# Performance work log

Hardware: AMD Instinct MI355X
Metric: run time of the kernel (lower is better)

The kernel has to match this reference:

```python
import jax, jax.numpy as jnp
import numpy as np

EMB_DIM = 512
N_HEAD = 8
EPS = 1e-5


def gen_pos_emb(emb_dim, max_len):
    half = emb_dim // 2
    r = 10000.0 ** (-1.0 / half)
    freq = r ** jnp.arange(half, dtype=jnp.float32)  # cumprod of [1, r, r, ...]
    phase = jnp.arange(max_len, dtype=jnp.float32)[:, None] * freq[None, :]  # [L, half]
    pe = jnp.zeros((max_len, emb_dim), dtype=jnp.float32)
    pe = pe.at[:, 0::2].set(jnp.sin(phase)).at[:, 1::2].set(jnp.cos(phase))
    return pe  # [L, E]


def setup_inputs() -> dict:
    key = jax.random.key(0)
    ks = jax.random.split(key, 12)
    bs, L, E, H, V = 8, 2048, EMB_DIM, N_HEAD, 32000
    inputs = jax.random.randint(ks[0], (bs, L), 0, V, dtype=jnp.int64 if jax.config.jax_enable_x64 else jnp.int32)
    lens = jnp.sort(jax.random.randint(ks[1], (bs,), 1, L + 1, dtype=jnp.int32))
    lens = lens.at[-1].set(L)  # model requires lens[-1] == max_len
    s = 0.02
    emb_table = (jax.random.normal(ks[2], (V, E), jnp.float32) * s).at[0].set(0.0)  # padding_idx=0
    qkv_w = jax.random.normal(ks[3], (3 * E, E), jnp.float32) * s
    qkv_b = jax.random.normal(ks[4], (3 * E,), jnp.float32) * s
    gn_w = jnp.ones((H,), jnp.float32)
    gn_b = jnp.zeros((H,), jnp.float32)
    ln_w = jnp.ones((E,), jnp.float32)
    ln_b = jnp.zeros((E,), jnp.float32)
    w1 = jax.random.normal(ks[5], (2 * E, E), jnp.float32) * s
    b1 = jax.random.normal(ks[6], (2 * E,), jnp.float32) * s
    w2 = jax.random.normal(ks[7], (E, 2 * E), jnp.float32) * s
    b2 = jax.random.normal(ks[8], (E,), jnp.float32) * s
    return {"inputs": inputs, "lens": lens, "emb_table": emb_table, "qkv_w": qkv_w,
            "qkv_b": qkv_b, "gn_w": gn_w, "gn_b": gn_b, "ln_w": ln_w, "ln_b": ln_b,
            "w1": w1, "b1": b1, "w2": w2, "b2": b2}


def _forward(inputs, lens, emb_table, qkv_w, qkv_b, gn_w, gn_b, ln_w, ln_b, w1, b1, w2, b2):
    bs, L = inputs.shape
    E, H = EMB_DIM, N_HEAD
    dh = E // H
    scaling = (E / H) ** -0.5

    # embedding + positional encoding; torch works seq-major: emb [L, bs, E]
    emb = emb_table[inputs.T] + gen_pos_emb(E, L)[:, None, :]

    # qkv projection and head split
    qkv = emb @ qkv_w.T + qkv_b                      # [L, bs, 3E]
    qkv = qkv.reshape(L, bs * H, 3 * dh).transpose(1, 0, 2)  # [B=bs*H, L, 3dh]
    q, k, v = jnp.split(qkv, 3, axis=-1)             # each [B, L, dh]

    # attention-sum: softmax over keys with zero-score mask, then sum over queries
    scores = jnp.einsum('bqd,bkd->bqk', q, k) * scaling   # [B, L, L]
    mask = scores == 0
    aw = jax.nn.softmax(jnp.where(mask, -jnp.inf, scores), axis=-1)
    aw = jnp.where(mask, 0.0, aw).sum(axis=-2)            # [B, L]

    attn_out = jnp.einsum('bl,bld->bd', aw, v).reshape(bs, H, dh)  # [bs, H, dh]

    # GroupNorm(n_head, n_head): per-channel normalization over dh with affine
    mu = attn_out.mean(-1, keepdims=True)
    var = attn_out.var(-1, keepdims=True)
    attn_out = (attn_out - mu) * jax.lax.rsqrt(var + EPS)
    attn_out = attn_out * gn_w[None, :, None] + gn_b[None, :, None]
    ft = attn_out.reshape(bs, E)

    # post_process: residual with length-normalized sum of embeddings
    x = ft + emb.sum(0) / lens.astype(emb.dtype)[:, None]  # [bs, E]

    # LayerNorm -> Linear -> tanh -> Linear, residual
    m = x.mean(-1, keepdims=True)
    vv = x.var(-1, keepdims=True)
    xn = (x - m) * jax.lax.rsqrt(vv + EPS) * ln_w + ln_b
    ff = jnp.tanh(xn @ w1.T + b1) @ w2.T + b2
    return x + ff


def reference(inputs, lens, emb_table, qkv_w, qkv_b, gn_w, gn_b, ln_w, ln_b, w1, b1, w2, b2):
    return _forward(inputs, lens, emb_table, qkv_w, qkv_b, gn_w, gn_b, ln_w, ln_b, w1, b1, w2, b2)
```

## Files before the change

kernel.cpp:

```cpp
#include <hip/hip_runtime.h>
#include <math.h>

#define L_SEQ 2048
#define BS 8
#define EMB 512
#define NHEAD 8
#define DH 64
#define NB (BS*NHEAD)

typedef short short8  __attribute__((ext_vector_type(8)));
typedef short short4v __attribute__((ext_vector_type(4)));
typedef float f32x4   __attribute__((ext_vector_type(4)));

__device__ __forceinline__ short f2bf(float x) {
    unsigned u = __float_as_uint(x);
    unsigned r = (u + 0x7FFFu + ((u >> 16) & 1u)) >> 16;
    return (short)r;
}
__device__ __forceinline__ float bf2f(short h) {
    return __uint_as_float(((unsigned)(unsigned short)h) << 16);
}

__global__ void freq_kernel(float* __restrict__ freq) {
    int j = threadIdx.x;
    double r = pow(10000.0, -1.0 / 256.0);
    float rf = (float)r;
    freq[j] = (float)pow((double)rf, (double)j);
}

__global__ __launch_bounds__(256) void pe_kernel(const float* __restrict__ freq,
                                                 float* __restrict__ pe) {
    int l = blockIdx.x;
    int j = threadIdx.x;
    float ph = (float)l * freq[j];
    pe[l*EMB + 2*j]     = sinf(ph);
    pe[l*EMB + 2*j + 1] = cosf(ph);
}

__global__ __launch_bounds__(256) void embed_kernel(const int* __restrict__ inputs,
                                                    const float* __restrict__ table,
                                                    const float* __restrict__ pe,
                                                    float* __restrict__ emb,
                                                    short* __restrict__ ahi,
                                                    short* __restrict__ alo) {
    int idx = blockIdx.x*256 + threadIdx.x;
    int e4 = idx & 127;
    int rb = idx >> 7;
    int b  = rb & 7;
    int l  = rb >> 3;
    int tok = inputs[b*L_SEQ + l];
    float4 tv = reinterpret_cast<const float4*>(table)[(size_t)tok*128 + e4];
    float4 pv = reinterpret_cast<const float4*>(pe)[(size_t)l*128 + e4];
    float4 o;
    o.x = tv.x + pv.x; o.y = tv.y + pv.y; o.z = tv.z + pv.z; o.w = tv.w + pv.w;
    reinterpret_cast<float4*>(emb)[(size_t)rb*128 + e4] = o;
    int e0   = e4 * 4;
    int tile = rb >> 4;
    int ks   = e0 >> 5;
    int lane = (rb & 15) + (((e0 >> 3) & 3) << 4);
    int j0   = e0 & 7;
    size_t off = ((((size_t)tile*16 + ks) << 6) + lane)*8 + j0;
    float v[4] = {o.x, o.y, o.z, o.w};
    short4v h4, l4;
    #pragma unroll
    for (int q = 0; q < 4; q++) {
        short hb = f2bf(v[q]);
        h4[q] = hb;
        l4[q] = f2bf(v[q] - bf2f(hb));
    }
    *reinterpret_cast<short4v*>(ahi + off) = h4;
    *reinterpret_cast<short4v*>(alo + off) = l4;
}

__global__ __launch_bounds__(256) void embsum_kernel(const float* __restrict__ emb,
                                                     float* __restrict__ embsum) {
    int b  = blockIdx.x;
    int ec = blockIdx.y;
    int lc = blockIdx.z;
    int e  = ec*256 + threadIdx.x;
    float s = 0.f;
    int l0 = lc*128;
    for (int l = l0; l < l0+128; l++)
        s += emb[((size_t)l*BS + b)*EMB + e];
    atomicAdd(&embsum[b*EMB + e], s);
}

__global__ __launch_bounds__(256) void wsplit_kernel(const float* __restrict__ src,
                                                     short8* __restrict__ hi,
                                                     short8* __restrict__ lo) {
    int idx = blockIdx.x*256 + threadIdx.x;
    int c = idx & 63;
    int r = idx >> 6;
    const float4* s4 = reinterpret_cast<const float4*>(src + (size_t)r*512 + c*8);
    float4 f0 = s4[0], f1 = s4[1];
    int ks   = c >> 2;
    int lane = (r & 15) + ((c & 3) << 4);
    int tile = r >> 4;
    float v[8] = {f0.x,f0.y,f0.z,f0.w,f1.x,f1.y,f1.z,f1.w};
    short8 h8, l8;
    #pragma unroll
    for (int q = 0; q < 8; q++) {
        short hb = f2bf(v[q]);
        h8[q] = hb;
        l8[q] = f2bf(v[q] - bf2f(hb));
    }
    size_t o = (((size_t)tile*16 + ks) << 6) + lane;
    hi[o] = h8; lo[o] = l8;
}

__global__ __launch_bounds__(256) void qkv_mfma_kernel(const short8* __restrict__ ahi,
                                                       const short8* __restrict__ alo,
                                                       const short8* __restrict__ bhi,
                                                       const short8* __restrict__ blo,
                                                       const float* __restrict__ bias,
                                                       short* __restrict__ qh,
                                                       short* __restrict__ kh,
                                                       float* __restrict__ vg) {
    __shared__ short8 sA[2][8][64];
    __shared__ short8 sB[2][8][64];
    int id  = blockIdx.x;
    int xcd = id & 7, pos = id >> 3;
    int nb  = pos % 12;
    int mb  = xcd*16 + pos/12;
    int t  = threadIdx.x;
    int w  = t >> 6, lane = t & 63;
    int wr = w >> 1, wc = w & 1;

    f32x4 acc[4][4];
    #pragma unroll
    for (int i = 0; i < 4; i++)
        #pragma unroll
        for (int j = 0; j < 4; j++)
            acc[i][j] = (f32x4){0.f, 0.f, 0.f, 0.f};

    short8 stg[8];
    #pragma unroll
    for (int i = 0; i < 8; i++) {
        int li = w*8 + i;
        int h = li & 1, ti = (li >> 1) & 7, isB = li >> 4;
        const short8* base = isB ? (h ? blo : bhi) : (h ? alo : ahi);
        int gt = isB ? (nb*8 + ti) : (mb*8 + ti);
        stg[i] = base[(((size_t)gt*16 + 0) << 6) + lane];
    }
    for (int ks = 0; ks < 16; ks++) {
        __syncthreads();
        #pragma unroll
        for (int i = 0; i < 8; i++) {
            int li = w*8 + i;
            int h = li & 1, ti = (li >> 1) & 7, isB = li >> 4;
            if (isB) sB[h][ti][lane] = stg[i];
            else     sA[h][ti][lane] = stg[i];
        }
        __syncthreads();
        if (ks < 15) {
            #pragma unroll
            for (int i = 0; i < 8; i++) {
                int li = w*8 + i;
                int h = li & 1, ti = (li >> 1) & 7, isB = li >> 4;
                const short8* base = isB ? (h ? blo : bhi) : (h ? alo : ahi);
                int gt = isB ? (nb*8 + ti) : (mb*8 + ti);
                stg[i] = base[(((size_t)gt*16 + (ks+1)) << 6) + lane];
            }
        }
        short8 Ah[4], Al[4];
        #pragma unroll
        for (int fi = 0; fi < 4; fi++) {
            Ah[fi] = sA[0][wr*4 + fi][lane];
            Al[fi] = sA[1][wr*4 + fi][lane];
        }
        #pragma unroll
        for (int fj = 0; fj < 4; fj++) {
            short8 Bh = sB[0][wc*4 + fj][lane];
            short8 Bl = sB[1][wc*4 + fj][lane];
            #pragma unroll
            for (int fi = 0; fi < 4; fi++) {
                acc[fi][fj] = __builtin_amdgcn_mfma_f32_16x16x32_bf16(Ah[fi], Bh, acc[fi][fj], 0, 0, 0);
                acc[fi][fj] = __builtin_amdgcn_mfma_f32_16x16x32_bf16(Ah[fi], Bl, acc[fi][fj], 0, 0, 0);
                acc[fi][fj] = __builtin_amdgcn_mfma_f32_16x16x32_bf16(Al[fi], Bh, acc[fi][fj], 0, 0, 0);
            }
        }
    }
    int row0 = (lane >> 4) * 4;
    int col  = lane & 15;
    #pragma unroll
    for (int fj = 0; fj < 4; fj++) {
        int n   = nb*128 + wc*64 + fj*16 + col;
        int h   = n / 192;
        int sel = (n % 192) / 64;
        float bn = bias[n];
        int nn = n & 63;
        #pragma unroll
        for (int fi = 0; fi < 4; fi++) {
            int m0 = mb*128 + wr*64 + fi*16 + row0;
            #pragma unroll
            for (int r = 0; r < 4; r++) {
                int m = m0 + r;
                int l = m >> 3, b = m & 7;
                size_t o = (((size_t)(b*NHEAD + h))*L_SEQ + l)*DH + nn;
                float val = acc[fi][fj][r] + bn;
                if (sel == 2)      vg[o] = val;
                else if (sel == 1) kh[o] = f2bf(val);
                else               qh[o] = f2bf(val);
            }
        }
    }
}

__global__ __launch_bounds__(256) void reformat16_kernel(const short* __restrict__ src,
                                                         short8* __restrict__ dst) {
    int idx = blockIdx.x*256 + threadIdx.x;
    int c  = idx & 7;
    int r  = (idx >> 3) & 2047;
    int bh = idx >> 14;
    short8 v = *reinterpret_cast<const short8*>(src + ((size_t)bh*L_SEQ + r)*DH + c*8);
    int ks   = c >> 2;
    int lane = (r & 15) + ((c & 3) << 4);
    int tile = r >> 4;
    dst[(((size_t)(bh*128 + tile)*2 + ks) << 6) + lane] = v;
}

__global__ __launch_bounds__(256) void ml_mfma_kernel(const short8* __restrict__ qbf,
                                                      const short8* __restrict__ kbf,
                                                      float* __restrict__ cq) {
    int bh = blockIdx.x, wv = threadIdx.x >> 6, lane = threadIdx.x & 63;
    int qt0 = (blockIdx.y*4 + wv)*4;
    short8 bq0[4], bq1[4];
    #pragma unroll
    for (int j = 0; j < 4; j++) {
        const short8* qp = qbf + (((size_t)(bh*128 + qt0 + j)*2) << 6) + lane;
        bq0[j] = qp[0]; bq1[j] = qp[64];
    }
    const short8* kp = kbf + ((size_t)bh << 14) + lane;
    float lsum[4] = {0.f, 0.f, 0.f, 0.f};
    for (int t = 0; t < 128; t++) {
        short8 a0 = kp[0], a1 = kp[64];
        kp += 128;
        #pragma unroll
        for (int j = 0; j < 4; j++) {
            f32x4 acc = {0.f, 0.f, 0.f, 0.f};
            acc = __builtin_amdgcn_mfma_f32_16x16x32_bf16(a0, bq0[j], acc, 0, 0, 0);
            acc = __builtin_amdgcn_mfma_f32_16x16x32_bf16(a1, bq1[j], acc, 0, 0, 0);
            #pragma unroll
            for (int r = 0; r < 4; r++)
                lsum[j] += (acc[r] != 0.f) ? __expf(acc[r]*0.125f) : 0.f;
        }
    }
    #pragma unroll
    for (int j = 0; j < 4; j++) {
        lsum[j] += __shfl_xor(lsum[j], 16);
        lsum[j] += __shfl_xor(lsum[j], 32);
    }
    if (lane < 16) {
        #pragma unroll
        for (int j = 0; j < 4; j++)
            cq[(size_t)bh*L_SEQ + (qt0+j)*16 + lane] = (lsum[j] > 0.f) ? 1.0f/lsum[j] : 0.f;
    }
}

__global__ __launch_bounds__(256) void kw_mfma_kernel(const short8* __restrict__ qbf,
                                                      const short8* __restrict__ kbf,
                                                      const float* __restrict__ cq,
                                                      float* __restrict__ wk) {
    int bh = blockIdx.x, wv = threadIdx.x >> 6, lane = threadIdx.x & 63;
    int kt0 = (blockIdx.y*4 + wv)*4;
    short8 bk0[4], bk1[4];
    #pragma unroll
    for (int j = 0; j < 4; j++) {
        const short8* kp = kbf + (((size_t)(bh*128 + kt0 + j)*2) << 6) + lane;
        bk0[j] = kp[0]; bk1[j] = kp[64];
    }
    const short8* qp = qbf + ((size_t)bh << 14) + lane;
    const float4* cp = reinterpret_cast<const float4*>(cq + (size_t)bh*L_SEQ) + (lane >> 4);
    float w[4] = {0.f, 0.f, 0.f, 0.f};
    for (int t = 0; t < 128; t++) {
        short8 a0 = qp[0], a1 = qp[64];
        qp += 128;
        float4 c4 = cp[0]; cp += 4;
        float cr[4] = {c4.x, c4.y, c4.z, c4.w};
        #pragma unroll
        for (int j = 0; j < 4; j++) {
            f32x4 acc = {0.f, 0.f, 0.f, 0.f};
            acc = __builtin_amdgcn_mfma_f32_16x16x32_bf16(a0, bk0[j], acc, 0, 0, 0);
            acc = __builtin_amdgcn_mfma_f32_16x16x32_bf16(a1, bk1[j], acc, 0, 0, 0);
            #pragma unroll
            for (int r = 0; r < 4; r++)
                w[j] += (acc[r] != 0.f) ? __expf(acc[r]*0.125f)*cr[r] : 0.f;
        }
    }
    #pragma unroll
    for (int j = 0; j < 4; j++) {
        w[j] += __shfl_xor(w[j], 16);
        w[j] += __shfl_xor(w[j], 32);
    }
    if (lane < 16) {
        #pragma unroll
        for (int j = 0; j < 4; j++)
            wk[(size_t)bh*L_SEQ + (kt0+j)*16 + lane] = w[j];
    }
}

__global__ __launch_bounds__(256) void pv_kernel(const float* __restrict__ vg,
                                                 const float* __restrict__ wk,
                                                 float* __restrict__ O) {
    __shared__ float red[256];
    int bidx = blockIdx.x;
    int seg  = blockIdx.y;
    int t    = threadIdx.x;
    int d    = t & 63;
    int ks   = t >> 6;
    const float* vrow = vg + ((size_t)bidx*L_SEQ + seg*256)*DH;
    const float* wrow = wk + (size_t)bidx*L_SEQ + seg*256;
    float acc = 0.f;
    for (int k = ks; k < 256; k += 4)
        acc += wrow[k] * vrow[k*64 + d];
    red[t] = acc;
    __syncthreads();
    if (t < 128) red[t] += red[t + 128];
    __syncthreads();
    if (t < 64) atomicAdd(&O[bidx*64 + t], red[t] + red[t + 64]);
}

__global__ __launch_bounds__(256) void ln_kernel(const float* __restrict__ O,
                                                 const float* __restrict__ embsum,
                                                 const int* __restrict__ lens,
                                                 const float* __restrict__ gn_w,
                                                 const float* __restrict__ gn_b,
                                                 const float* __restrict__ ln_w,
                                                 const float* __restrict__ ln_b,
                                                 float* __restrict__ xbuf,
                                                 float* __restrict__ xnbuf) {
    int b = blockIdx.x;
    int t = threadIdx.x;
    __shared__ float x[EMB];
    __shared__ float rbuf[16];
    {
        int h = t >> 5;
        int i32 = t & 31;
        float v0 = O[b*EMB + h*64 + i32];
        float v1 = O[b*EMB + h*64 + i32 + 32];
        float s = v0+v1, ss = v0*v0 + v1*v1;
        #pragma unroll
        for (int off = 16; off >= 1; off >>= 1) {
            s  += __shfl_xor(s,  off, 32);
            ss += __shfl_xor(ss, off, 32);
        }
        float mu  = s * (1.f/64.f);
        float var = ss * (1.f/64.f) - mu*mu;
        float rstd = rsqrtf(var + 1e-5f);
        float gw = gn_w[h], gb = gn_b[h];
        float len = (float)lens[b];
        x[h*64+i32]    = (v0-mu)*rstd*gw + gb + embsum[b*EMB + h*64+i32] / len;
        x[h*64+i32+32] = (v1-mu)*rstd*gw + gb + embsum[b*EMB + h*64+i32+32] / len;
    }
    __syncthreads();
    float xv0 = x[t], xv1 = x[t+256];
    {
        float s = xv0+xv1, ss = xv0*xv0 + xv1*xv1;
        #pragma unroll
        for (int off = 32; off >= 1; off >>= 1) {
            s  += __shfl_xor(s,  off);
            ss += __shfl_xor(ss, off);
        }
        int wid = t >> 6;
        if ((t & 63) == 0) { rbuf[wid] = s; rbuf[8+wid] = ss; }
        __syncthreads();
        float S  = rbuf[0]+rbuf[1]+rbuf[2]+rbuf[3];
        float SS = rbuf[8]+rbuf[9]+rbuf[10]+rbuf[11];
        float mu  = S * (1.f/512.f);
        float var = SS * (1.f/512.f) - mu*mu;
        float rstd = rsqrtf(var + 1e-5f);
        xnbuf[b*EMB + t]       = (xv0-mu)*rstd*ln_w[t]     + ln_b[t];
        xnbuf[b*EMB + t + 256] = (xv1-mu)*rstd*ln_w[t+256] + ln_b[t+256];
        xbuf[b*EMB + t]        = xv0;
        xbuf[b*EMB + t + 256]  = xv1;
    }
}

__global__ __launch_bounds__(256) void mlp1_kernel(const float* __restrict__ xnbuf,
                                                   const float* __restrict__ w1,
                                                   const float* __restrict__ b1,
                                                   float* __restrict__ h1buf) {
    __shared__ float sxn[BS][EMB];
    int t = threadIdx.x;
    #pragma unroll
    for (int i = 0; i < 4; i++)
        reinterpret_cast<float4*>(&sxn[0][0])[t + 256*i] =
            reinterpret_cast<const float4*>(xnbuf)[t + 256*i];
    __syncthreads();
    int b = t & 7;
    int j = blockIdx.x*32 + (t >> 3);
    const float4* wr = reinterpret_cast<const float4*>(w1 + (size_t)j*512);
    const float4* xr = reinterpret_cast<const float4*>(&sxn[b][0]);
    float a0 = 0.f, a1 = 0.f;
    #pragma unroll 8
    for (int i = 0; i < 128; i += 2) {
        float4 wv = wr[i],   xv = xr[i];
        a0 += wv.x*xv.x + wv.y*xv.y + wv.z*xv.z + wv.w*xv.w;
        float4 wv1 = wr[i+1], xv1 = xr[i+1];
        a1 += wv1.x*xv1.x + wv1.y*xv1.y + wv1.z*xv1.z + wv1.w*xv1.w;
    }
    h1buf[b*1024 + j] = tanhf(a0 + a1 + b1[j]);
}

__global__ __launch_bounds__(256) void mlp2_kernel(const float* __restrict__ h1buf,
                                                   const float* __restrict__ xbuf,
                                                   const float* __restrict__ w2,
                                                   const float* __restrict__ b2,
                                                   float* __restrict__ out) {
    __shared__ float sh1[BS][2*EMB];
    int t = threadIdx.x;
    #pragma unroll
    for (int i = 0; i < 8; i++)
        reinterpret_cast<float4*>(&sh1[0][0])[t + 256*i] =
            reinterpret_cast<const float4*>(h1buf)[t + 256*i];
    __syncthreads();
    int b = t & 7;
    int e = blockIdx.x*32 + (t >> 3);
    const float4* wr = reinterpret_cast<const float4*>(w2 + (size_t)e*1024);
    const float4* hr = reinterpret_cast<const float4*>(&sh1[b][0]);
    float a0 = 0.f, a1 = 0.f;
    #pragma unroll 8
    for (int i = 0; i < 256; i += 2) {
        float4 wv = wr[i],   hv = hr[i];
        a0 += wv.x*hv.x + wv.y*hv.y + wv.z*hv.z + wv.w*hv.w;
        float4 wv1 = wr[i+1], hv1 = hr[i+1];
        a1 += wv1.x*hv1.x + wv1.y*hv1.y + wv1.z*hv1.z + wv1.w*hv1.w;
    }
    out[b*EMB + e] = xbuf[b*EMB + e] + a0 + a1 + b2[e];
}

extern "C" void kernel_launch(void* const* d_in, const int* in_sizes, int n_in,
                              void* d_out, int out_size, void* d_ws, size_t ws_size,
                              hipStream_t stream) {
    const int*   inputs    = (const int*)d_in[0];
    const int*   lens      = (const int*)d_in[1];
    const float* emb_table = (const float*)d_in[2];
    const float* qkv_w     = (const float*)d_in[3];
    const float* qkv_b     = (const float*)d_in[4];
    const float* gn_w      = (const float*)d_in[5];
    const float* gn_b      = (const float*)d_in[6];
    const float* ln_w      = (const float*)d_in[7];
    const float* ln_b      = (const float*)d_in[8];
    const float* w1        = (const float*)d_in[9];
    const float* b1        = (const float*)d_in[10];
    const float* w2        = (const float*)d_in[11];
    const float* b2        = (const float*)d_in[12];
    float* out = (float*)d_out;

    float* ws = (float*)d_ws;
    const size_t NE = (size_t)L_SEQ*BS*EMB;
    float* emb    = ws;
    float* vg     = emb + NE;
    float* pe     = vg  + NE;
    float* afrag  = pe  + (size_t)L_SEQ*EMB;
    short* ahi_s  = reinterpret_cast<short*>(afrag);
    short* alo_s  = ahi_s + NE;
    float* qkrows = afrag + NE;
    short* qh     = reinterpret_cast<short*>(qkrows);
    short* kh     = qh + NE;
    float* wfrag  = qkrows + NE;
    short8* bhi   = reinterpret_cast<short8*>(wfrag);
    short8* blo   = bhi + 98304;
    float* cqbuf  = wfrag + 786432;
    float* wkbuf  = cqbuf + (size_t)NB*L_SEQ;
    float* freq   = wkbuf + (size_t)NB*L_SEQ;
    float* embsum = freq + 256;
    float* Oacc   = embsum + BS*EMB;
    float* xbuf   = Oacc + NB*DH;
    float* xnbuf  = xbuf + BS*EMB;
    float* h1buf  = xnbuf + BS*EMB;
    short8* kbf = reinterpret_cast<short8*>(emb);
    short8* qbf = kbf + (size_t)NB*128*2*64;

    hipMemsetAsync(embsum, 0, 2*BS*EMB*sizeof(float), stream);

    freq_kernel<<<1, 256, 0, stream>>>(freq);
    pe_kernel<<<L_SEQ, 256, 0, stream>>>(freq, pe);
    embed_kernel<<<(L_SEQ*BS*(EMB/4))/256, 256, 0, stream>>>(inputs, emb_table, pe, emb,
                                                             ahi_s, alo_s);
    embsum_kernel<<<dim3(BS, 2, 16), 256, 0, stream>>>(emb, embsum);
    wsplit_kernel<<<384, 256, 0, stream>>>(qkv_w, bhi, blo);
    qkv_mfma_kernel<<<1536, 256, 0, stream>>>(reinterpret_cast<const short8*>(ahi_s),
                                              reinterpret_cast<const short8*>(alo_s),
                                              bhi, blo, qkv_b, qh, kh, vg);
    reformat16_kernel<<<4096, 256, 0, stream>>>(kh, kbf);
    reformat16_kernel<<<4096, 256, 0, stream>>>(qh, qbf);
    ml_mfma_kernel<<<dim3(NB, 8), 256, 0, stream>>>(qbf, kbf, cqbuf);
    kw_mfma_kernel<<<dim3(NB, 8), 256, 0, stream>>>(qbf, kbf, cqbuf, wkbuf);
    pv_kernel<<<dim3(NB, 8), 256, 0, stream>>>(vg, wkbuf, Oacc);
    ln_kernel<<<BS, 256, 0, stream>>>(Oacc, embsum, lens, gn_w, gn_b, ln_w, ln_b, xbuf, xnbuf);
    mlp1_kernel<<<32, 256, 0, stream>>>(xnbuf, w1, b1, h1buf);
    mlp2_kernel<<<16, 256, 0, stream>>>(h1buf, xbuf, w2, b2, out);
}
```

Before: 465.1 us.

## Split attention key loops across two blocks, fold scale into Q, use exp2

Result: faster. 422.4 us (-9.2%).

```diff
diff --git a/kernel.cpp b/kernel.cpp
--- a/kernel.cpp
+++ b/kernel.cpp
@@ -7,6 +7,7 @@
 #define NHEAD 8
 #define DH 64
 #define NB (BS*NHEAD)
+#define SCALE_Q 0.18033688f
 
 typedef short short8  __attribute__((ext_vector_type(8)));
 typedef short short4v __attribute__((ext_vector_type(4)));
@@ -200,7 +201,7 @@
                 float val = acc[fi][fj][r] + bn;
                 if (sel == 2)      vg[o] = val;
                 else if (sel == 1) kh[o] = f2bf(val);
-                else               qh[o] = f2bf(val);
+                else               qh[o] = f2bf(val * SCALE_Q);
             }
         }
     }
@@ -223,6 +224,7 @@
                                                       const short8* __restrict__ kbf,
                                                       float* __restrict__ cq) {
     int bh = blockIdx.x, wv = threadIdx.x >> 6, lane = threadIdx.x & 63;
+    int z  = blockIdx.z;
     int qt0 = (blockIdx.y*4 + wv)*4;
     short8 bq0[4], bq1[4];
     #pragma unroll
@@ -230,9 +232,9 @@
         const short8* qp = qbf + (((size_t)(bh*128 + qt0 + j)*2) << 6) + lane;
         bq0[j] = qp[0]; bq1[j] = qp[64];
     }
-    const short8* kp = kbf + ((size_t)bh << 14) + lane;
+    const short8* kp = kbf + ((size_t)bh << 14) + lane + (size_t)z*64*128;
     float lsum[4] = {0.f, 0.f, 0.f, 0.f};
-    for (int t = 0; t < 128; t++) {
+    for (int t = 0; t < 64; t++) {
         short8 a0 = kp[0], a1 = kp[64];
         kp += 128;
         #pragma unroll
@@ -242,7 +244,7 @@
             acc = __builtin_amdgcn_mfma_f32_16x16x32_bf16(a1, bq1[j], acc, 0, 0, 0);
             #pragma unroll
             for (int r = 0; r < 4; r++)
-                lsum[j] += (acc[r] != 0.f) ? __expf(acc[r]*0.125f) : 0.f;
+                lsum[j] += (acc[r] != 0.f) ? __builtin_amdgcn_exp2f(acc[r]) : 0.f;
         }
     }
     #pragma unroll
@@ -253,7 +255,7 @@
     if (lane < 16) {
         #pragma unroll
         for (int j = 0; j < 4; j++)
-            cq[(size_t)bh*L_SEQ + (qt0+j)*16 + lane] = (lsum[j] > 0.f) ? 1.0f/lsum[j] : 0.f;
+            atomicAdd(&cq[(size_t)bh*L_SEQ + (qt0+j)*16 + lane], lsum[j]);
     }
 }
 
@@ -262,6 +264,7 @@
                                                       const float* __restrict__ cq,
                                                       float* __restrict__ wk) {
     int bh = blockIdx.x, wv = threadIdx.x >> 6, lane = threadIdx.x & 63;
+    int z  = blockIdx.z;
     int kt0 = (blockIdx.y*4 + wv)*4;
     short8 bk0[4], bk1[4];
     #pragma unroll
@@ -269,22 +272,28 @@
         const short8* kp = kbf + (((size_t)(bh*128 + kt0 + j)*2) << 6) + lane;
         bk0[j] = kp[0]; bk1[j] = kp[64];
     }
-    const short8* qp = qbf + ((size_t)bh << 14) + lane;
-    const float4* cp = reinterpret_cast<const float4*>(cq + (size_t)bh*L_SEQ) + (lane >> 4);
+    const short8* qp = qbf + ((size_t)bh << 14) + lane + (size_t)z*64*128;
+    const float4* cp = reinterpret_cast<const float4*>(cq + (size_t)bh*L_SEQ) + (lane >> 4) + z*64*4;
     float w[4] = {0.f, 0.f, 0.f, 0.f};
-    for (int t = 0; t < 128; t++) {
+    for (int t = 0; t < 64; t++) {
         short8 a0 = qp[0], a1 = qp[64];
         qp += 128;
         float4 c4 = cp[0]; cp += 4;
-        float cr[4] = {c4.x, c4.y, c4.z, c4.w};
+        float cr[4];
+        cr[0] = (c4.x > 0.f) ? __builtin_amdgcn_rcpf(c4.x) : 0.f;
+        cr[1] = (c4.y > 0.f) ? __builtin_amdgcn_rcpf(c4.y) : 0.f;
+        cr[2] = (c4.z > 0.f) ? __builtin_amdgcn_rcpf(c4.z) : 0.f;
+        cr[3] = (c4.w > 0.f) ? __builtin_amdgcn_rcpf(c4.w) : 0.f;
         #pragma unroll
         for (int j = 0; j < 4; j++) {
             f32x4 acc = {0.f, 0.f, 0.f, 0.f};
             acc = __builtin_amdgcn_mfma_f32_16x16x32_bf16(a0, bk0[j], acc, 0, 0, 0);
             acc = __builtin_amdgcn_mfma_f32_16x16x32_bf16(a1, bk1[j], acc, 0, 0, 0);
             #pragma unroll
-            for (int r = 0; r < 4; r++)
-                w[j] += (acc[r] != 0.f) ? __expf(acc[r]*0.125f)*cr[r] : 0.f;
+            for (int r = 0; r < 4; r++) {
+                float p = __builtin_amdgcn_exp2f(acc[r]);
+                w[j] += (acc[r] != 0.f) ? p*cr[r] : 0.f;
+            }
         }
     }
     #pragma unroll
@@ -295,7 +304,7 @@
     if (lane < 16) {
         #pragma unroll
         for (int j = 0; j < 4; j++)
-            wk[(size_t)bh*L_SEQ + (kt0+j)*16 + lane] = w[j];
+            atomicAdd(&wk[(size_t)bh*L_SEQ + (kt0+j)*16 + lane], w[j]);
     }
 }
 
@@ -473,6 +482,7 @@
     short8* qbf = kbf + (size_t)NB*128*2*64;
 
     hipMemsetAsync(embsum, 0, 2*BS*EMB*sizeof(float), stream);
+    hipMemsetAsync(cqbuf, 0, 2*(size_t)NB*L_SEQ*sizeof(float), stream);
 
     freq_kernel<<<1, 256, 0, stream>>>(freq);
     pe_kernel<<<L_SEQ, 256, 0, stream>>>(freq, pe);
@@ -485,8 +495,8 @@
                                               bhi, blo, qkv_b, qh, kh, vg);
     reformat16_kernel<<<4096, 256, 0, stream>>>(kh, kbf);
     reformat16_kernel<<<4096, 256, 0, stream>>>(qh, qbf);
-    ml_mfma_kernel<<<dim3(NB, 8), 256, 0, stream>>>(qbf, kbf, cqbuf);
-    kw_mfma_kernel<<<dim3(NB, 8), 256, 0, stream>>>(qbf, kbf, cqbuf, wkbuf);
+    ml_mfma_kernel<<<dim3(NB, 8, 2), 256, 0, stream>>>(qbf, kbf, cqbuf);
+    kw_mfma_kernel<<<dim3(NB, 8, 2), 256, 0, stream>>>(qbf, kbf, cqbuf, wkbuf);
     pv_kernel<<<dim3(NB, 8), 256, 0, stream>>>(vg, wkbuf, Oacc);
     ln_kernel<<<BS, 256, 0, stream>>>(Oacc, embsum, lens, gn_w, gn_b, ln_w, ln_b, xbuf, xnbuf);
     mlp1_kernel<<<32, 256, 0, stream>>>(xnbuf, w1, b1, h1buf);
```
